# Kernel optimization log

Measured on AMD Instinct MI355X. Metric: run time of the kernel, lower is better.

## Reference

```python
import jax, jax.numpy as jnp
import numpy as np

DIM = 512
DEPTH = 6
HEADS = 8
HD = DIM // HEADS          # head dim = 64
HALF = HD // 4             # rope half_dim = 16
MLP_H = int(DIM * 4.0)
TOKENS = [1, 4, 16, 64]    # CLS, S1, S2, S3
N = sum(TOKENS)            # 85
MAX_FREQ = 10.0
BATCH = 1024
LN_EPS = 1e-5


def _build_mask():
    # CLS sees CLS+S3; each scale sees CLS+itself (block-diagonal + CLS column)
    m = np.full((N, N), -np.inf, dtype=np.float32)
    cum = np.cumsum([0] + TOKENS)  # [0,1,5,21,85]
    m[0, 0] = 0.0
    m[0, cum[3]:cum[4]] = 0.0
    for i in range(1, 4):
        s, e = cum[i], cum[i + 1]
        m[s:e, 0] = 0.0
        m[s:e, s:e] = 0.0
    return jnp.asarray(m)

MASK = _build_mask()
FREQS = jnp.exp(jnp.arange(HALF, dtype=jnp.float32) * (-np.log(MAX_FREQ) / HALF))


def _layer_norm(x, g, b):
    mu = x.mean(-1, keepdims=True)
    var = ((x - mu) ** 2).mean(-1, keepdims=True)
    return (x - mu) * jax.lax.rsqrt(var + LN_EPS) * g + b


def _rope2d(t, coords):
    # t: [B,H,P,HD], coords: [P,2] in [0,1]^2
    ang_x = coords[:, 0:1] * FREQS[None, :] * (2.0 * jnp.pi)  # [P,HALF]
    ang_y = coords[:, 1:2] * FREQS[None, :] * (2.0 * jnp.pi)
    cx, sx = jnp.cos(ang_x), jnp.sin(ang_x)
    cy, sy = jnp.cos(ang_y), jnp.sin(ang_y)
    B, H, P, _ = t.shape
    t = t.reshape(B, H, P, 4, HALF)
    x0, x1, x2, x3 = t[..., 0, :], t[..., 1, :], t[..., 2, :], t[..., 3, :]
    r = jnp.stack([x0 * cx - x1 * sx,
                   x0 * sx + x1 * cx,
                   x2 * cy - x3 * sy,
                   x2 * sy + x3 * cy], axis=3)
    return r.reshape(B, H, P, HD)


def _rope_skip_cls(t, coords):
    return jnp.concatenate([t[:, :, :1], _rope2d(t[:, :, 1:], coords)], axis=2)


def _block(x, coords, p):
    (ln1g, ln1b, qkvw, qkvb, projw, projb,
     ln2g, ln2b, f1w, f1b, f2w, f2b) = p
    B, Nn, D = x.shape
    h = _layer_norm(x, ln1g, ln1b)
    qkv = h @ qkvw + qkvb                         # [B,N,3D]
    qkv = qkv.reshape(B, Nn, 3, HEADS, HD).transpose(2, 0, 3, 1, 4)
    q, k, v = qkv[0], qkv[1], qkv[2]              # [B,H,N,HD]
    q = _rope_skip_cls(q, coords)
    k = _rope_skip_cls(k, coords)
    attn = jnp.einsum('bhqd,bhkd->bhqk', q, k) * (HD ** -0.5) + MASK
    attn = jax.nn.softmax(attn, axis=-1)
    out = jnp.einsum('bhqk,bhkd->bhqd', attn, v)
    out = out.transpose(0, 2, 1, 3).reshape(B, Nn, D)
    x = x + (out @ projw + projb)
    h = _layer_norm(x, ln2g, ln2b)
    h = jax.nn.gelu(h @ f1w + f1b, approximate=False) @ f2w + f2b
    return x + h


def setup_inputs() -> dict:
    key = jax.random.key(0)
    ks = jax.random.split(key, 8)
    s = 0.02
    nrm = lambda k, shape: jax.random.normal(k, shape, jnp.float32) * s
    return dict(
        x=jax.random.normal(ks[0], (BATCH, N, DIM), jnp.float32),
        coords=jax.random.uniform(ks[1], (N - 1, 2), jnp.float32),
        ln1_g=jnp.ones((DEPTH, DIM), jnp.float32),
        ln1_b=jnp.zeros((DEPTH, DIM), jnp.float32),
        qkv_w=nrm(ks[2], (DEPTH, DIM, 3 * DIM)),
        qkv_b=jnp.zeros((DEPTH, 3 * DIM), jnp.float32),
        proj_w=nrm(ks[3], (DEPTH, DIM, DIM)),
        proj_b=jnp.zeros((DEPTH, DIM), jnp.float32),
        ln2_g=jnp.ones((DEPTH, DIM), jnp.float32),
        ln2_b=jnp.zeros((DEPTH, DIM), jnp.float32),
        fc1_w=nrm(ks[4], (DEPTH, DIM, MLP_H)),
        fc1_b=jnp.zeros((DEPTH, MLP_H), jnp.float32),
        fc2_w=nrm(ks[5], (DEPTH, MLP_H, DIM)),
        fc2_b=jnp.zeros((DEPTH, DIM), jnp.float32),
    )


def reference(x, coords, ln1_g, ln1_b, qkv_w, qkv_b, proj_w, proj_b,
              ln2_g, ln2_b, fc1_w, fc1_b, fc2_w, fc2_b):
    for i in range(DEPTH):
        x = _block(x, coords,
                   (ln1_g[i], ln1_b[i], qkv_w[i], qkv_b[i], proj_w[i], proj_b[i],
                    ln2_g[i], ln2_b[i], fc1_w[i], fc1_b[i], fc2_w[i], fc2_b[i]))
    return x
```

## Files before the change

### kernel.cpp

```cpp
#include <hip/hip_runtime.h>
#include <hip/hip_bf16.h>
#include <math.h>

#define DIMX 512
#define NTOK 85
#define BATCH 1024
#define M_ROWS (BATCH * NTOK)
#define MLP_H 2048
#define DEPTH 6

typedef __attribute__((ext_vector_type(8))) short short8;
typedef __attribute__((ext_vector_type(4))) float f32x4;

__device__ inline float bf2f(ushort u) {
    union { unsigned int i; float f; } v; v.i = ((unsigned int)u) << 16; return v.f;
}
__device__ inline ushort f2bf(float f) {
    __hip_bfloat16 h = __float2bfloat16(f);
    union { __hip_bfloat16 h; ushort u; } v; v.h = h; return v.u;
}
__device__ inline unsigned int pack2(float a, float b) {
    return (unsigned int)f2bf(a) | ((unsigned int)f2bf(b) << 16);
}
__device__ inline float gelu_fast(float v) {
    float u = 1.5957691f * fmaf(0.044715f * v, v * v, v);
    return v / (1.0f + __expf(-u));
}

__device__ inline void gload16(const ushort* g, ushort* lds) {
    __builtin_amdgcn_global_load_lds(
        (const __attribute__((address_space(1))) unsigned int*)g,
        (__attribute__((address_space(3))) unsigned int*)lds, 16, 0, 0);
}

__global__ __launch_bounds__(256) void transpose_bf16(const float* __restrict__ in,
                                                      ushort* __restrict__ out,
                                                      int K, int N) {
    __shared__ float tile[32][33];
    int n0 = blockIdx.x * 32, k0 = blockIdx.y * 32;
    int tx = threadIdx.x, ty = threadIdx.y;
    #pragma unroll
    for (int j = 0; j < 32; j += 8)
        tile[ty + j][tx] = in[(size_t)(k0 + ty + j) * N + n0 + tx];
    __syncthreads();
    #pragma unroll
    for (int j = 0; j < 32; j += 8)
        out[(size_t)(n0 + ty + j) * K + k0 + tx] = f2bf(tile[tx][ty + j]);
}

__global__ void rope_table(const float* __restrict__ coords, float* __restrict__ tab) {
    int t = blockIdx.x;
    int idx = threadIdx.x;
    float freq = expf(-(float)idx * (2.302585093f / 16.0f));
    float twopi = 6.283185307179586f;
    float ax = coords[t * 2 + 0] * freq * twopi;
    float ay = coords[t * 2 + 1] * freq * twopi;
    tab[t * 64 + idx]      = cosf(ax);
    tab[t * 64 + 16 + idx] = sinf(ax);
    tab[t * 64 + 32 + idx] = cosf(ay);
    tab[t * 64 + 48 + idx] = sinf(ay);
}

__global__ __launch_bounds__(256) void ln_kernel(const float* __restrict__ x,
                                                 const float* __restrict__ g,
                                                 const float* __restrict__ bta,
                                                 ushort* __restrict__ out) {
    int w = threadIdx.x >> 6, lane = threadIdx.x & 63;
    size_t row = (size_t)blockIdx.x * 4 + w;
    const float* xr = x + row * DIMX;
    int c = lane * 8;
    float4 v0 = *(const float4*)(xr + c);
    float4 v1 = *(const float4*)(xr + c + 4);
    float s = v0.x + v0.y + v0.z + v0.w + v1.x + v1.y + v1.z + v1.w;
    #pragma unroll
    for (int m = 32; m; m >>= 1) s += __shfl_xor(s, m);
    float mu = s * (1.0f / 512.0f);
    float d0 = v0.x - mu, d1 = v0.y - mu, d2 = v0.z - mu, d3 = v0.w - mu;
    float d4 = v1.x - mu, d5 = v1.y - mu, d6 = v1.z - mu, d7 = v1.w - mu;
    float q = d0*d0 + d1*d1 + d2*d2 + d3*d3 + d4*d4 + d5*d5 + d6*d6 + d7*d7;
    #pragma unroll
    for (int m = 32; m; m >>= 1) q += __shfl_xor(q, m);
    float rs = rsqrtf(q * (1.0f / 512.0f) + 1e-5f);
    float4 g0 = *(const float4*)(g + c), g1 = *(const float4*)(g + c + 4);
    float4 b0 = *(const float4*)(bta + c), b1 = *(const float4*)(bta + c + 4);
    uint4 o;
    o.x = pack2(d0 * rs * g0.x + b0.x, d1 * rs * g0.y + b0.y);
    o.y = pack2(d2 * rs * g0.z + b0.z, d3 * rs * g0.w + b0.w);
    o.z = pack2(d4 * rs * g1.x + b1.x, d5 * rs * g1.y + b1.y);
    o.w = pack2(d6 * rs * g1.z + b1.z, d7 * rs * g1.w + b1.w);
    *(uint4*)&out[row * DIMX + c] = o;
}

template <int EPI>
__global__ __launch_bounds__(256, 2) void gemm_wide(const ushort* __restrict__ A,
                                                    const ushort* __restrict__ Bt,
                                                    const float* __restrict__ bias,
                                                    float* __restrict__ outF,
                                                    ushort* __restrict__ outB,
                                                    int M, int N, int K,
                                                    const float* __restrict__ tab) {
    __shared__ ushort AsF[3 * 8192] __attribute__((aligned(16)));
    __shared__ ushort BsF[3 * 4096] __attribute__((aligned(16)));
    int tid = threadIdx.x;
    int w = tid >> 6, lane = tid & 63;
    int wm2 = (w >> 1) * 128;
    int wn = (w & 1) * 64;

    int nbx = gridDim.x;
    int nwg = nbx * gridDim.y;
    int orig = blockIdx.y * nbx + blockIdx.x;
    int q8 = nwg >> 3, r8 = nwg & 7;
    int xcd = orig & 7, loc = orig >> 3;
    int id = (xcd < r8) ? xcd * (q8 + 1) + loc : r8 * (q8 + 1) + (xcd - r8) * q8 + loc;
    int m0 = (id / nbx) * 256;
    int n0 = (id % nbx) * 128;

    int srow = tid >> 2;
    int scol = ((tid & 3) ^ ((srow >> 1) & 3)) * 8;
    int rA0 = m0 + srow;       if (rA0 >= M) rA0 = M - 1;
    int rA1 = m0 + 64 + srow;  if (rA1 >= M) rA1 = M - 1;
    int rA2 = m0 + 128 + srow; if (rA2 >= M) rA2 = M - 1;
    int rA3 = m0 + 192 + srow; if (rA3 >= M) rA3 = M - 1;
    const ushort* gA0 = A + (size_t)rA0 * K + scol;
    const ushort* gA1 = A + (size_t)rA1 * K + scol;
    const ushort* gA2 = A + (size_t)rA2 * K + scol;
    const ushort* gA3 = A + (size_t)rA3 * K + scol;
    const ushort* gB0 = Bt + (size_t)(n0 + srow) * K + scol;
    const ushort* gB1 = Bt + (size_t)(n0 + 64 + srow) * K + scol;
    int dwz = w * 512;
    int swA = 0, swB = 0;

#define STAGEW() do {                                                          \
        gload16(gA0, &AsF[swA + dwz]);                                         \
        gload16(gA1, &AsF[swA + 2048 + dwz]);                                  \
        gload16(gA2, &AsF[swA + 4096 + dwz]);                                  \
        gload16(gA3, &AsF[swA + 6144 + dwz]);                                  \
        gload16(gB0, &BsF[swB + dwz]);                                         \
        gload16(gB1, &BsF[swB + 2048 + dwz]);                                  \
        gA0 += 32; gA1 += 32; gA2 += 32; gA3 += 32; gB0 += 32; gB1 += 32;      \
        swA += 8192; if (swA == 24576) swA = 0;                                \
        swB += 4096; if (swB == 12288) swB = 0; } while (0)

    int l15 = lane & 15, lq = lane >> 4;
    int sw = (lq ^ ((l15 >> 1) & 3)) * 8;
    int aoff = (wm2 + l15) * 32 + sw;
    int boff = (wn + l15) * 32 + sw;
    int roffA = 0, roffB = 0;

    int NT = K >> 5;

    STAGEW(); STAGEW();

    f32x4 acc[8][4] = {};

    for (int t = 0; t < NT; ++t) {
        if (t < NT - 1) asm volatile("s_waitcnt vmcnt(6)" ::: "memory");
        else            asm volatile("s_waitcnt vmcnt(0)" ::: "memory");
        __builtin_amdgcn_s_barrier();
        short8 a[8], b[4];
        #pragma unroll
        for (int i = 0; i < 8; i++) a[i] = *(const short8*)&AsF[roffA + aoff + i * 512];
        #pragma unroll
        for (int j = 0; j < 4; j++) b[j] = *(const short8*)&BsF[roffB + boff + j * 512];
        if (t + 2 < NT) STAGEW();
        asm volatile("s_waitcnt lgkmcnt(0)" ::: "memory");
        __builtin_amdgcn_sched_barrier(0);
        __builtin_amdgcn_s_setprio(1);
        #pragma unroll
        for (int i = 0; i < 8; i++)
            #pragma unroll
            for (int j = 0; j < 4; j++)
                acc[i][j] = __builtin_amdgcn_mfma_f32_16x16x32_bf16(a[i], b[j], acc[i][j], 0, 0, 0);
        __builtin_amdgcn_s_setprio(0);
        roffA += 8192; if (roffA == 24576) roffA = 0;
        roffB += 4096; if (roffB == 12288) roffB = 0;
    }
#undef STAGEW

    int cr = lq * 4;
    int cc = l15;
    if (EPI == 0) {
        bool ropeReg = (n0 + wn) < 1024;
        int gnb = n0 + wn + cc;
        float bb0 = bias[gnb], bb1 = bias[gnb + 16], bb2 = bias[gnb + 32], bb3 = bias[gnb + 48];
        #pragma unroll
        for (int i = 0; i < 8; i++) {
            #pragma unroll
            for (int rr = 0; rr < 4; rr++) {
                int gm = m0 + wm2 + i * 16 + cr + rr;
                if (gm >= M) continue;
                int n = gm % NTOK;
                float v0 = acc[i][0][rr] + bb0;
                float v1 = acc[i][1][rr] + bb1;
                float v2 = acc[i][2][rr] + bb2;
                float v3 = acc[i][3][rr] + bb3;
                if (ropeReg && n > 0) {
                    const float* tt = tab + (size_t)(n - 1) * 64 + cc;
                    float cx = tt[0], sx = tt[16], cy = tt[32], sy = tt[48];
                    float y0 = v0 * cx - v1 * sx;
                    float y1 = v0 * sx + v1 * cx;
                    float y2 = v2 * cy - v3 * sy;
                    float y3 = v2 * sy + v3 * cy;
                    v0 = y0; v1 = y1; v2 = y2; v3 = y3;
                }
                size_t o = (size_t)gm * N + gnb;
                outB[o]      = f2bf(v0);
                outB[o + 16] = f2bf(v1);
                outB[o + 32] = f2bf(v2);
                outB[o + 48] = f2bf(v3);
            }
        }
    } else {
        #pragma unroll
        for (int i = 0; i < 8; i++) {
            #pragma unroll
            for (int rr = 0; rr < 4; rr++) {
                int gm = m0 + wm2 + i * 16 + cr + rr;
                if (gm >= M) continue;
                #pragma unroll
                for (int j = 0; j < 4; j++) {
                    int gn = n0 + wn + j * 16 + cc;
                    float v = acc[i][j][rr] + bias[gn];
                    size_t o = (size_t)gm * N + gn;
                    if (EPI == 1) {
                        outF[o] = outF[o] + v;
                    } else {
                        outB[o] = f2bf(gelu_fast(v));
                    }
                }
            }
        }
    }
}

__global__ __launch_bounds__(384) void attn_kernel(const ushort* __restrict__ qkv,
                                                   ushort* __restrict__ out) {
    __shared__ ushort SU[13824] __attribute__((aligned(16)));
    __shared__ ushort Vt[6656]  __attribute__((aligned(16)));
    int bh = blockIdx.x;
    int b = bh >> 3, h = bh & 7;
    int tid = threadIdx.x;
    size_t base = (size_t)b * NTOK * 1536 + h * 64;

    for (int it = tid; it < 1536; it += 384) {
        int mat = (it >= 768) ? 1 : 0;
        int item = it - mat * 768;
        int n = item >> 3, g = item & 7;
        short8 v = {};
        if (n < NTOK)
            v = *(const short8*)&qkv[base + (size_t)n * 1536 + mat * 512 + g * 8];
        *(short8*)&SU[mat * 6912 + n * 72 + g * 8] = v;
    }
    for (int it = tid; it < 768; it += 384) {
        int n = it % 96;
        int d0 = (it / 96) * 8;
        short8 v = {};
        if (n < NTOK)
            v = *(const short8*)&qkv[base + (size_t)n * 1536 + 1024 + d0];
        #pragma unroll
        for (int j = 0; j < 8; j++)
            Vt[(d0 + j) * 104 + n] = (ushort)v[j];
    }
    __syncthreads();

    int wid = tid >> 6;
    int lane = tid & 63;
    int q = lane >> 4, c = lane & 15;
    int i0 = wid * 16;

    f32x4 acc[6] = {};
    #pragma unroll
    for (int kk = 0; kk < 2; kk++) {
        short8 aq = *(const short8*)&SU[(i0 + c) * 72 + kk * 32 + q * 8];
        #pragma unroll
        for (int t = 0; t < 6; t++) {
            short8 bk = *(const short8*)&SU[6912 + (t * 16 + c) * 72 + kk * 32 + q * 8];
            acc[t] = __builtin_amdgcn_mfma_f32_16x16x32_bf16(aq, bk, acc[t], 0, 0, 0);
        }
    }
    __syncthreads();

    #pragma unroll
    for (int r = 0; r < 4; r++) {
        int i = i0 + q * 4 + r;
        int si = (i == 0) ? 3 : (i < 5 ? 1 : (i < 21 ? 2 : 3));
        float vs[6];
        float m = -1e30f;
        #pragma unroll
        for (int t = 0; t < 6; t++) {
            int j = t * 16 + c;
            int sj = (j == 0) ? si : (j < 5 ? 1 : (j < 21 ? 2 : (j < NTOK ? 3 : -1)));
            float v = (sj == si) ? acc[t][r] * 0.125f : -1e30f;
            vs[t] = v;
            m = fmaxf(m, v);
        }
        #pragma unroll
        for (int mk = 8; mk; mk >>= 1) m = fmaxf(m, __shfl_xor(m, mk));
        float s = 0.f, ps[6];
        #pragma unroll
        for (int t = 0; t < 6; t++) { ps[t] = __expf(vs[t] - m); s += ps[t]; }
        #pragma unroll
        for (int mk = 8; mk; mk >>= 1) s += __shfl_xor(s, mk);
        float inv = 1.0f / s;
        #pragma unroll
        for (int t = 0; t < 6; t++)
            SU[i * 104 + t * 16 + c] = f2bf(ps[t] * inv);
    }
    __syncthreads();

    f32x4 o2[4] = {};
    #pragma unroll
    for (int kk = 0; kk < 3; kk++) {
        short8 ap = *(const short8*)&SU[(i0 + c) * 104 + kk * 32 + q * 8];
        #pragma unroll
        for (int nt = 0; nt < 4; nt++) {
            short8 bv = *(const short8*)&Vt[(nt * 16 + c) * 104 + kk * 32 + q * 8];
            o2[nt] = __builtin_amdgcn_mfma_f32_16x16x32_bf16(ap, bv, o2[nt], 0, 0, 0);
        }
    }
    size_t orow = (size_t)b * NTOK;
    #pragma unroll
    for (int nt = 0; nt < 4; nt++) {
        #pragma unroll
        for (int r = 0; r < 4; r++) {
            int i = i0 + q * 4 + r;
            if (i < NTOK)
                out[(orow + i) * DIMX + h * 64 + nt * 16 + c] = f2bf(o2[nt][r]);
        }
    }
}

extern "C" void kernel_launch(void* const* d_in, const int* in_sizes, int n_in,
                              void* d_out, int out_size, void* d_ws, size_t ws_size,
                              hipStream_t stream) {
    const float* x_in    = (const float*)d_in[0];
    const float* coords  = (const float*)d_in[1];
    const float* ln1_g   = (const float*)d_in[2];
    const float* ln1_b   = (const float*)d_in[3];
    const float* qkv_w   = (const float*)d_in[4];
    const float* qkv_b   = (const float*)d_in[5];
    const float* proj_w  = (const float*)d_in[6];
    const float* proj_b  = (const float*)d_in[7];
    const float* ln2_g   = (const float*)d_in[8];
    const float* ln2_b   = (const float*)d_in[9];
    const float* fc1_w   = (const float*)d_in[10];
    const float* fc1_b   = (const float*)d_in[11];
    const float* fc2_w   = (const float*)d_in[12];
    const float* fc2_b   = (const float*)d_in[13];

    char* ws = (char*)d_ws;
    size_t off = 0;
    auto alloc = [&](size_t bytes) -> void* {
        void* p = ws + off;
        off += (bytes + 255) & ~(size_t)255;
        return p;
    };
    auto asz = [](size_t b) { return (b + 255) & ~(size_t)255; };

    const size_t WPL = 512 * 1536 + 512 * 512 + 512 * 2048 + 2048 * 512;

    size_t fixed = asz(WPL * DEPTH * sizeof(ushort)) + asz(84 * 64 * sizeof(float));
    int Bc = 1024;
    while (Bc > 4) {
        size_t rc = (size_t)Bc * NTOK;
        size_t need = fixed + asz(rc * DIMX * sizeof(ushort)) + asz(rc * MLP_H * sizeof(ushort));
        if (need <= ws_size) break;
        Bc >>= 1;
    }
    size_t Rc = (size_t)Bc * NTOK;

    ushort* wt   = (ushort*)alloc(WPL * DEPTH * sizeof(ushort));
    float*  tab  = (float*)alloc(84 * 64 * sizeof(float));
    ushort* hbuf = (ushort*)alloc(Rc * DIMX * sizeof(ushort));
    ushort* big  = (ushort*)alloc(Rc * MLP_H * sizeof(ushort));

    hipMemcpyAsync(d_out, x_in, (size_t)M_ROWS * DIMX * sizeof(float),
                   hipMemcpyDeviceToDevice, stream);

    rope_table<<<84, 16, 0, stream>>>(coords, tab);

    dim3 tb(32, 8);
    for (int l = 0; l < DEPTH; l++) {
        ushort* wl = wt + (size_t)l * WPL;
        transpose_bf16<<<dim3(1536 / 32, 512 / 32), tb, 0, stream>>>(
            qkv_w + (size_t)l * 512 * 1536, wl, 512, 1536);
        transpose_bf16<<<dim3(512 / 32, 512 / 32), tb, 0, stream>>>(
            proj_w + (size_t)l * 512 * 512, wl + 786432, 512, 512);
        transpose_bf16<<<dim3(2048 / 32, 512 / 32), tb, 0, stream>>>(
            fc1_w + (size_t)l * 512 * 2048, wl + 1048576, 512, 2048);
        transpose_bf16<<<dim3(512 / 32, 2048 / 32), tb, 0, stream>>>(
            fc2_w + (size_t)l * 2048 * 512, wl + 2097152, 2048, 512);
    }

    int mt256 = (int)(Rc / 256);
    int lnblocks = (int)(Rc / 4);
    for (int c = 0; c < BATCH / Bc; c++) {
        float* xc = (float*)d_out + (size_t)c * Rc * DIMX;
        int Mc = (int)Rc;
        for (int l = 0; l < DEPTH; l++) {
            ushort* wl = wt + (size_t)l * WPL;
            ln_kernel<<<lnblocks, 256, 0, stream>>>(
                xc, ln1_g + l * 512, ln1_b + l * 512, hbuf);
            gemm_wide<0><<<dim3(1536 / 128, mt256), 256, 0, stream>>>(
                hbuf, wl, qkv_b + (size_t)l * 1536, nullptr, big, Mc, 1536, 512, tab);
            attn_kernel<<<Bc * 8, 384, 0, stream>>>(big, hbuf);
            gemm_wide<1><<<dim3(512 / 128, mt256), 256, 0, stream>>>(
                hbuf, wl + 786432, proj_b + (size_t)l * 512, xc, nullptr,
                Mc, 512, 512, nullptr);
            ln_kernel<<<lnblocks, 256, 0, stream>>>(
                xc, ln2_g + l * 512, ln2_b + l * 512, hbuf);
            gemm_wide<2><<<dim3(2048 / 128, mt256), 256, 0, stream>>>(
                hbuf, wl + 1048576, fc1_b + (size_t)l * 2048, nullptr, big,
                Mc, 2048, 512, nullptr);
            gemm_wide<1><<<dim3(512 / 128, mt256), 256, 0, stream>>>(
                big, wl + 2097152, fc2_b + (size_t)l * 512, xc, nullptr,
                Mc, 512, 2048, nullptr);
        }
    }
}
```

Baseline: 7.141 ms.

## Load GEMM B fragments directly from global into double-buffered registers

```diff
diff --git a/kernel.cpp b/kernel.cpp
--- a/kernel.cpp
+++ b/kernel.cpp
@@ -100,7 +100,6 @@
                                                     int M, int N, int K,
                                                     const float* __restrict__ tab) {
     __shared__ ushort AsF[3 * 8192] __attribute__((aligned(16)));
-    __shared__ ushort BsF[3 * 4096] __attribute__((aligned(16)));
     int tid = threadIdx.x;
     int w = tid >> 6, lane = tid & 63;
     int wm2 = (w >> 1) * 128;
@@ -125,57 +124,94 @@
     const ushort* gA1 = A + (size_t)rA1 * K + scol;
     const ushort* gA2 = A + (size_t)rA2 * K + scol;
     const ushort* gA3 = A + (size_t)rA3 * K + scol;
-    const ushort* gB0 = Bt + (size_t)(n0 + srow) * K + scol;
-    const ushort* gB1 = Bt + (size_t)(n0 + 64 + srow) * K + scol;
     int dwz = w * 512;
-    int swA = 0, swB = 0;
-
-#define STAGEW() do {                                                          \
+    int swA = 0;
+
+#define STAGE_A() do {                                                         \
         gload16(gA0, &AsF[swA + dwz]);                                         \
         gload16(gA1, &AsF[swA + 2048 + dwz]);                                  \
         gload16(gA2, &AsF[swA + 4096 + dwz]);                                  \
         gload16(gA3, &AsF[swA + 6144 + dwz]);                                  \
-        gload16(gB0, &BsF[swB + dwz]);                                         \
-        gload16(gB1, &BsF[swB + 2048 + dwz]);                                  \
-        gA0 += 32; gA1 += 32; gA2 += 32; gA3 += 32; gB0 += 32; gB1 += 32;      \
-        swA += 8192; if (swA == 24576) swA = 0;                                \
-        swB += 4096; if (swB == 12288) swB = 0; } while (0)
+        gA0 += 32; gA1 += 32; gA2 += 32; gA3 += 32;                            \
+        swA += 8192; if (swA == 24576) swA = 0; } while (0)
 
     int l15 = lane & 15, lq = lane >> 4;
     int sw = (lq ^ ((l15 >> 1) & 3)) * 8;
     int aoff = (wm2 + l15) * 32 + sw;
-    int boff = (wn + l15) * 32 + sw;
-    int roffA = 0, roffB = 0;
+    int roffA = 0;
+
+    const ushort* bp = Bt + (size_t)(n0 + wn + l15) * K + lq * 8;
+    const int bstep = 16 * K;
 
     int NT = K >> 5;
 
-    STAGEW(); STAGEW();
+    STAGE_A(); STAGE_A();
+    short8 bA0 = *(const short8*)(bp);
+    short8 bA1 = *(const short8*)(bp + bstep);
+    short8 bA2 = *(const short8*)(bp + 2 * bstep);
+    short8 bA3 = *(const short8*)(bp + 3 * bstep);
+    short8 bB0, bB1, bB2, bB3;
+    bp += 32;
 
     f32x4 acc[8][4] = {};
 
-    for (int t = 0; t < NT; ++t) {
-        if (t < NT - 1) asm volatile("s_waitcnt vmcnt(6)" ::: "memory");
-        else            asm volatile("s_waitcnt vmcnt(0)" ::: "memory");
-        __builtin_amdgcn_s_barrier();
-        short8 a[8], b[4];
-        #pragma unroll
-        for (int i = 0; i < 8; i++) a[i] = *(const short8*)&AsF[roffA + aoff + i * 512];
-        #pragma unroll
-        for (int j = 0; j < 4; j++) b[j] = *(const short8*)&BsF[roffB + boff + j * 512];
-        if (t + 2 < NT) STAGEW();
-        asm volatile("s_waitcnt lgkmcnt(0)" ::: "memory");
-        __builtin_amdgcn_sched_barrier(0);
-        __builtin_amdgcn_s_setprio(1);
-        #pragma unroll
-        for (int i = 0; i < 8; i++)
-            #pragma unroll
-            for (int j = 0; j < 4; j++)
-                acc[i][j] = __builtin_amdgcn_mfma_f32_16x16x32_bf16(a[i], b[j], acc[i][j], 0, 0, 0);
-        __builtin_amdgcn_s_setprio(0);
-        roffA += 8192; if (roffA == 24576) roffA = 0;
-        roffB += 4096; if (roffB == 12288) roffB = 0;
-    }
-#undef STAGEW
+    for (int t = 0; t < NT; t += 2) {
+        {
+            const int T = t;
+            if (T < NT - 1) asm volatile("s_waitcnt vmcnt(8)" ::: "memory");
+            else            asm volatile("s_waitcnt vmcnt(4)" ::: "memory");
+            __builtin_amdgcn_s_barrier();
+            __builtin_amdgcn_sched_barrier(0);
+            if (T + 2 < NT) STAGE_A();
+            bB0 = *(const short8*)(bp);
+            bB1 = *(const short8*)(bp + bstep);
+            bB2 = *(const short8*)(bp + 2 * bstep);
+            bB3 = *(const short8*)(bp + 3 * bstep);
+            bp += 32;
+            short8 a[8];
+            #pragma unroll
+            for (int i = 0; i < 8; i++) a[i] = *(const short8*)&AsF[roffA + aoff + i * 512];
+            __builtin_amdgcn_s_setprio(1);
+            #pragma unroll
+            for (int i = 0; i < 8; i++) {
+                acc[i][0] = __builtin_amdgcn_mfma_f32_16x16x32_bf16(a[i], bA0, acc[i][0], 0, 0, 0);
+                acc[i][1] = __builtin_amdgcn_mfma_f32_16x16x32_bf16(a[i], bA1, acc[i][1], 0, 0, 0);
+                acc[i][2] = __builtin_amdgcn_mfma_f32_16x16x32_bf16(a[i], bA2, acc[i][2], 0, 0, 0);
+                acc[i][3] = __builtin_amdgcn_mfma_f32_16x16x32_bf16(a[i], bA3, acc[i][3], 0, 0, 0);
+            }
+            __builtin_amdgcn_s_setprio(0);
+            roffA += 8192; if (roffA == 24576) roffA = 0;
+        }
+        {
+            const int T = t + 1;
+            if (T < NT - 1) asm volatile("s_waitcnt vmcnt(8)" ::: "memory");
+            else            asm volatile("s_waitcnt vmcnt(4)" ::: "memory");
+            __builtin_amdgcn_s_barrier();
+            __builtin_amdgcn_sched_barrier(0);
+            if (T + 2 < NT) STAGE_A();
+            if (T + 1 < NT) {
+                bA0 = *(const short8*)(bp);
+                bA1 = *(const short8*)(bp + bstep);
+                bA2 = *(const short8*)(bp + 2 * bstep);
+                bA3 = *(const short8*)(bp + 3 * bstep);
+                bp += 32;
+            }
+            short8 a[8];
+            #pragma unroll
+            for (int i = 0; i < 8; i++) a[i] = *(const short8*)&AsF[roffA + aoff + i * 512];
+            __builtin_amdgcn_s_setprio(1);
+            #pragma unroll
+            for (int i = 0; i < 8; i++) {
+                acc[i][0] = __builtin_amdgcn_mfma_f32_16x16x32_bf16(a[i], bB0, acc[i][0], 0, 0, 0);
+                acc[i][1] = __builtin_amdgcn_mfma_f32_16x16x32_bf16(a[i], bB1, acc[i][1], 0, 0, 0);
+                acc[i][2] = __builtin_amdgcn_mfma_f32_16x16x32_bf16(a[i], bB2, acc[i][2], 0, 0, 0);
+                acc[i][3] = __builtin_amdgcn_mfma_f32_16x16x32_bf16(a[i], bB3, acc[i][3], 0, 0, 0);
+            }
+            __builtin_amdgcn_s_setprio(0);
+            roffA += 8192; if (roffA == 24576) roffA = 0;
+        }
+    }
+#undef STAGE_A
 
     int cr = lq * 4;
     int cc = l15;
```

Result: slower. 8.894 ms (+24.5%).
